# Performance work log

Measured on AMD Instinct MI355X. Metric: run time of the kernel, lower is better.

## Reference

```python
import jax, jax.numpy as jnp
import numpy as np

B = 16384
N_NEIGH = 50
D = 64
NUM_USERS = 100000
NUM_ITEMS = 100000
NUM_ENTITIES = 200000


def setup_inputs() -> dict:
    key = jax.random.key(0)
    ks = jax.random.split(key, 16)
    s = 1.0 / np.sqrt(D)
    return {
        "user_indices": jax.random.randint(ks[0], (B,), 0, NUM_USERS),
        "item_indices": jax.random.randint(ks[1], (B,), 0, NUM_ITEMS),
        "kg_adj_batch": jax.random.randint(ks[2], (B, N_NEIGH), 0, NUM_ENTITIES),
        "user_table": jax.random.normal(ks[3], (NUM_USERS, D), jnp.float32),
        "item_table": jax.random.normal(ks[4], (NUM_ITEMS, D), jnp.float32),
        "entity_table": jax.random.normal(ks[5], (NUM_ENTITIES, D), jnp.float32),
        "attn_W": jax.random.normal(ks[6], (2 * D, 1), jnp.float32) * s,
        "attn_b": jnp.zeros((1,), jnp.float32),
        "kg_W1": jax.random.normal(ks[7], (D, D), jnp.float32) * s,
        "kg_b1": jnp.zeros((D,), jnp.float32),
        "kg_W2": jax.random.normal(ks[8], (D, D), jnp.float32) * s,
        "kg_b2": jnp.zeros((D,), jnp.float32),
        "comb_W": jax.random.normal(ks[9], (2 * D, D), jnp.float32) * s,
        "comb_b": jnp.zeros((D,), jnp.float32),
        "out_W": jax.random.normal(ks[10], (2 * D, 1), jnp.float32) * s,
        "out_b": jnp.zeros((1,), jnp.float32),
    }


def reference(user_indices, item_indices, kg_adj_batch,
              user_table, item_table, entity_table,
              attn_W, attn_b, kg_W1, kg_b1, kg_W2, kg_b2,
              comb_W, comb_b, out_W, out_b):
    user_emb = user_table[user_indices]          # [B, D]
    item_emb = item_table[item_indices]          # [B, D]
    nbr_idx = jnp.clip(kg_adj_batch, 0)
    neighbor_emb = entity_table[nbr_idx]         # [B, N, D]
    # attention_linear(cat([item, nbr])) == item @ Wi + nbr @ Wn + b (avoids [B,N,2D])
    Wi, Wn = attn_W[:D], attn_W[D:]
    attn_scores = item_emb @ Wi + jnp.einsum('bnd,do->bno', neighbor_emb, Wn)[..., 0] + attn_b  # [B, N]
    attn_scores = jax.nn.leaky_relu(attn_scores, negative_slope=0.2)
    attn_weights = jax.nn.softmax(attn_scores, axis=1)                 # softmax over neighbors
    neighbor_attn = jnp.einsum('bn,bnd->bd', attn_weights, neighbor_emb)
    refined_kg = jax.nn.relu(neighbor_attn @ kg_W1 + kg_b1) @ kg_W2 + kg_b2
    combined_item = jnp.concatenate([item_emb, refined_kg], axis=1)
    final_item_rep = jax.nn.relu(combined_item @ comb_W + comb_b)      # dropout = identity (eval)
    combined_user_item = jnp.concatenate([user_emb, final_item_rep], axis=1)
    score = (combined_user_item @ out_W + out_b)[:, 0]
    return score
```

## Files before the change

### kernel.cpp

```cpp
#include <hip/hip_runtime.h>

#define NN 50
#define D 64
#define GRP 10

typedef unsigned int uint32;
typedef unsigned short ushort16;

__device__ __forceinline__ float wave_sum64(float x) {
#pragma unroll
  for (int off = 32; off > 0; off >>= 1)
    x += __shfl_xor(x, off, 64);
  return x;
}

__device__ __forceinline__ float readlane_f(float v, int l) {
  return __uint_as_float(__builtin_amdgcn_readlane(__float_as_uint(v), l));
}

__device__ __forceinline__ ushort16 f32_to_bf16(float f) {
  uint32 u = __float_as_uint(f);
  u += 0x7FFF + ((u >> 16) & 1);
  return (ushort16)(u >> 16);
}

__global__ __launch_bounds__(256, 4) void ent_proj(
    const float* __restrict__ ent_tab, const float* __restrict__ attn_W,
    float* __restrict__ proj, ushort16* __restrict__ ent_bf, int rows)
{
  const int  lane = threadIdx.x & 63;
  const long wave = (long)blockIdx.x * 4 + (threadIdx.x >> 6);
  const long base = wave * GRP;
  if (base >= rows) return;
  const float Wn = attn_W[D + lane];
  float v[GRP];
#pragma unroll
  for (int i = 0; i < GRP; ++i) {
    long r = base + i; if (r > rows - 1) r = rows - 1;
    v[i] = ent_tab[r * D + lane];
  }
  float s[GRP];
#pragma unroll
  for (int i = 0; i < GRP; ++i)
    s[i] = wave_sum64(v[i] * Wn);
#pragma unroll
  for (int i = 0; i < GRP; ++i) {
    const long r = base + i;
    if (r < rows) ent_bf[r * D + lane] = f32_to_bf16(v[i]);
  }
  if (lane == 0) {
#pragma unroll
    for (int i = 0; i < GRP; ++i)
      if (base + i < rows) proj[base + i] = s[i];
  }
}

#define PGRP 5

__device__ __forceinline__ void load_pair_grp(uint32 (&buf)[PGRP],
                                              const int* __restrict__ adjb,
                                              const uint32* __restrict__ ent32,
                                              int g, int half, int sub) {
#pragma unroll
  for (int i = 0; i < PGRP; ++i) {
    const int p = g * PGRP + i;
    int t0 = adjb[2 * p + 0]; t0 = t0 < 0 ? 0 : t0;
    int t1 = adjb[2 * p + 1]; t1 = t1 < 0 ? 0 : t1;
    const int t = half ? t1 : t0;
    buf[i] = ent32[(size_t)t * 32 + sub];
  }
}

__device__ __forceinline__ void acc_pair_grp(const uint32 (&buf)[PGRP],
                                             float e, int g, int half,
                                             float& lo0, float& lo1,
                                             float& hi0, float& hi1) {
#pragma unroll
  for (int i = 0; i < PGRP; ++i) {
    const int p = g * PGRP + i;
    const float w0 = readlane_f(e, 2 * p + 0);
    const float w1 = readlane_f(e, 2 * p + 1);
    const float w  = half ? w1 : w0;
    const float lo = __uint_as_float(buf[i] << 16);
    const float hi = __uint_as_float(buf[i] & 0xFFFF0000u);
    if (i & 1) { lo1 = fmaf(w, lo, lo1); hi1 = fmaf(w, hi, hi1); }
    else       { lo0 = fmaf(w, lo, lo0); hi0 = fmaf(w, hi, hi0); }
  }
}

__global__ __launch_bounds__(256, 4) void kgat_attn2(
    const int* __restrict__ item_idx, const int* __restrict__ adj,
    const float* __restrict__ item_tab,
    const uint32* __restrict__ ent32, const float* __restrict__ proj,
    const float* __restrict__ attn_W, const float* __restrict__ attn_b,
    float* __restrict__ naws, int B)
{
  const int lane = threadIdx.x & 63;
  const int wv   = threadIdx.x >> 6;
  const int b    = blockIdx.x * 4 + wv;
  if (b >= B) return;
  const int half = lane >> 5;
  const int sub  = lane & 31;

  const int* adjb = adj + (long)b * NN;

  uint32 GA[PGRP], GB[PGRP];
  load_pair_grp(GA, adjb, ent32, 0, half, sub);
  load_pair_grp(GB, adjb, ent32, 1, half, sub);

  const float item = item_tab[(long)item_idx[b] * D + lane];
  const float base = wave_sum64(item * attn_W[lane]) + attn_b[0];

  const int myn = lane < NN ? lane : NN - 1;
  int mi = adjb[myn]; mi = mi < 0 ? 0 : mi;
  float s = proj[mi] + base;
  s = s > 0.f ? s : 0.2f * s;
  const float e = (lane < NN) ? __expf(s - 8.0f) : 0.f;
  const float denom = wave_sum64(e);

  float lo0 = 0.f, lo1 = 0.f, hi0 = 0.f, hi1 = 0.f;
  acc_pair_grp(GA, e, 0, half, lo0, lo1, hi0, hi1);
  load_pair_grp(GA, adjb, ent32, 2, half, sub);
  acc_pair_grp(GB, e, 1, half, lo0, lo1, hi0, hi1);
  load_pair_grp(GB, adjb, ent32, 3, half, sub);
  acc_pair_grp(GA, e, 2, half, lo0, lo1, hi0, hi1);
  load_pair_grp(GA, adjb, ent32, 4, half, sub);
  acc_pair_grp(GB, e, 3, half, lo0, lo1, hi0, hi1);
  acc_pair_grp(GA, e, 4, half, lo0, lo1, hi0, hi1);

  float nlo = lo0 + lo1;
  float nhi = hi0 + hi1;
  nlo += __shfl_xor(nlo, 32, 64);
  nhi += __shfl_xor(nhi, 32, 64);

  const float inv = 1.0f / denom;
  if (lane < 32) {
    float2 val = make_float2(nlo * inv, nhi * inv);
    *(float2*)(naws + (long)b * D + 2 * sub) = val;
  }
}

__global__ __launch_bounds__(256, 4) void kgat_mlp4(
    const int* __restrict__ user_idx, const int* __restrict__ item_idx,
    const float* __restrict__ user_tab, const float* __restrict__ item_tab,
    const float* __restrict__ naws,
    const float* __restrict__ W1, const float* __restrict__ b1,
    const float* __restrict__ W2, const float* __restrict__ b2,
    const float* __restrict__ cW, const float* __restrict__ cb,
    const float* __restrict__ oW, const float* __restrict__ ob,
    float* __restrict__ out, int B)
{
  __shared__ __align__(16) float s_a[4 * 4 * D];
  __shared__ __align__(16) float s_i[4 * 4 * D];

  const int lane = threadIdx.x & 63;
  const int wv   = threadIdx.x >> 6;
  const int b0   = (blockIdx.x * 4 + wv) * 4;
  if (b0 >= B) return;

  float* saA = s_a + (wv * 4 + 0) * D;
  float* saB = s_a + (wv * 4 + 1) * D;
  float* saC = s_a + (wv * 4 + 2) * D;
  float* saD = s_a + (wv * 4 + 3) * D;
  float* siA = s_i + (wv * 4 + 0) * D;
  float* siB = s_i + (wv * 4 + 1) * D;
  float* siC = s_i + (wv * 4 + 2) * D;
  float* siD = s_i + (wv * 4 + 3) * D;

  const int bA = b0 + 0 < B ? b0 + 0 : B - 1;
  const int bB = b0 + 1 < B ? b0 + 1 : B - 1;
  const int bC = b0 + 2 < B ? b0 + 2 : B - 1;
  const int bD = b0 + 3 < B ? b0 + 3 : B - 1;

  saA[lane] = naws[(long)bA * D + lane];
  saB[lane] = naws[(long)bB * D + lane];
  saC[lane] = naws[(long)bC * D + lane];
  saD[lane] = naws[(long)bD * D + lane];
  siA[lane] = item_tab[(long)item_idx[bA] * D + lane];
  siB[lane] = item_tab[(long)item_idx[bB] * D + lane];
  siC[lane] = item_tab[(long)item_idx[bC] * D + lane];
  siD[lane] = item_tab[(long)item_idx[bD] * D + lane];
  const float usA = user_tab[(long)user_idx[bA] * D + lane];
  const float usB = user_tab[(long)user_idx[bB] * D + lane];
  const float usC = user_tab[(long)user_idx[bC] * D + lane];
  const float usD = user_tab[(long)user_idx[bD] * D + lane];

  const float b1v = b1[lane];
  float hA0 = b1v, hA1 = 0.f, hB0 = b1v, hB1 = 0.f;
  float hC0 = b1v, hC1 = 0.f, hD0 = b1v, hD1 = 0.f;
#pragma unroll
  for (int d = 0; d < D; d += 4) {
    const float w0 = W1[(d + 0) * D + lane];
    const float w1 = W1[(d + 1) * D + lane];
    const float w2 = W1[(d + 2) * D + lane];
    const float w3 = W1[(d + 3) * D + lane];
    const float4 cA = *(const float4*)(saA + d);
    const float4 cB = *(const float4*)(saB + d);
    const float4 cC = *(const float4*)(saC + d);
    const float4 cD = *(const float4*)(saD + d);
    hA0 = fmaf(cA.x, w0, hA0); hA1 = fmaf(cA.y, w1, hA1);
    hA0 = fmaf(cA.z, w2, hA0); hA1 = fmaf(cA.w, w3, hA1);
    hB0 = fmaf(cB.x, w0, hB0); hB1 = fmaf(cB.y, w1, hB1);
    hB0 = fmaf(cB.z, w2, hB0); hB1 = fmaf(cB.w, w3, hB1);
    hC0 = fmaf(cC.x, w0, hC0); hC1 = fmaf(cC.y, w1, hC1);
    hC0 = fmaf(cC.z, w2, hC0); hC1 = fmaf(cC.w, w3, hC1);
    hD0 = fmaf(cD.x, w0, hD0); hD1 = fmaf(cD.y, w1, hD1);
    hD0 = fmaf(cD.z, w2, hD0); hD1 = fmaf(cD.w, w3, hD1);
  }
  saA[lane] = fmaxf(hA0 + hA1, 0.f);
  saB[lane] = fmaxf(hB0 + hB1, 0.f);
  saC[lane] = fmaxf(hC0 + hC1, 0.f);
  saD[lane] = fmaxf(hD0 + hD1, 0.f);

  const float b2v = b2[lane];
  float rA0 = b2v, rA1 = 0.f, rB0 = b2v, rB1 = 0.f;
  float rC0 = b2v, rC1 = 0.f, rD0 = b2v, rD1 = 0.f;
#pragma unroll
  for (int d = 0; d < D; d += 4) {
    const float w0 = W2[(d + 0) * D + lane];
    const float w1 = W2[(d + 1) * D + lane];
    const float w2 = W2[(d + 2) * D + lane];
    const float w3 = W2[(d + 3) * D + lane];
    const float4 cA = *(const float4*)(saA + d);
    const float4 cB = *(const float4*)(saB + d);
    const float4 cC = *(const float4*)(saC + d);
    const float4 cD = *(const float4*)(saD + d);
    rA0 = fmaf(cA.x, w0, rA0); rA1 = fmaf(cA.y, w1, rA1);
    rA0 = fmaf(cA.z, w2, rA0); rA1 = fmaf(cA.w, w3, rA1);
    rB0 = fmaf(cB.x, w0, rB0); rB1 = fmaf(cB.y, w1, rB1);
    rB0 = fmaf(cB.z, w2, rB0); rB1 = fmaf(cB.w, w3, rB1);
    rC0 = fmaf(cC.x, w0, rC0); rC1 = fmaf(cC.y, w1, rC1);
    rC0 = fmaf(cC.z, w2, rC0); rC1 = fmaf(cC.w, w3, rC1);
    rD0 = fmaf(cD.x, w0, rD0); rD1 = fmaf(cD.y, w1, rD1);
    rD0 = fmaf(cD.z, w2, rD0); rD1 = fmaf(cD.w, w3, rD1);
  }
  saA[lane] = rA0 + rA1;
  saB[lane] = rB0 + rB1;
  saC[lane] = rC0 + rC1;
  saD[lane] = rD0 + rD1;

  const float cbv = cb[lane];
  float fA0 = cbv, fA1 = 0.f, fB0 = cbv, fB1 = 0.f;
  float fC0 = cbv, fC1 = 0.f, fD0 = cbv, fD1 = 0.f;
#pragma unroll
  for (int k = 0; k < D; k += 4) {
    const float w0 = cW[(k + 0) * D + lane];
    const float w1 = cW[(k + 1) * D + lane];
    const float w2 = cW[(k + 2) * D + lane];
    const float w3 = cW[(k + 3) * D + lane];
    const float4 cA = *(const float4*)(siA + k);
    const float4 cB = *(const float4*)(siB + k);
    const float4 cC = *(const float4*)(siC + k);
    const float4 cD = *(const float4*)(siD + k);
    fA0 = fmaf(cA.x, w0, fA0); fA1 = fmaf(cA.y, w1, fA1);
    fA0 = fmaf(cA.z, w2, fA0); fA1 = fmaf(cA.w, w3, fA1);
    fB0 = fmaf(cB.x, w0, fB0); fB1 = fmaf(cB.y, w1, fB1);
    fB0 = fmaf(cB.z, w2, fB0); fB1 = fmaf(cB.w, w3, fB1);
    fC0 = fmaf(cC.x, w0, fC0); fC1 = fmaf(cC.y, w1, fC1);
    fC0 = fmaf(cC.z, w2, fC0); fC1 = fmaf(cC.w, w3, fC1);
    fD0 = fmaf(cD.x, w0, fD0); fD1 = fmaf(cD.y, w1, fD1);
    fD0 = fmaf(cD.z, w2, fD0); fD1 = fmaf(cD.w, w3, fD1);
  }
#pragma unroll
  for (int k = 0; k < D; k += 4) {
    const float w0 = cW[(D + k + 0) * D + lane];
    const float w1 = cW[(D + k + 1) * D + lane];
    const float w2 = cW[(D + k + 2) * D + lane];
    const float w3 = cW[(D + k + 3) * D + lane];
    const float4 cA = *(const float4*)(saA + k);
    const float4 cB = *(const float4*)(saB + k);
    const float4 cC = *(const float4*)(saC + k);
    const float4 cD = *(const float4*)(saD + k);
    fA0 = fmaf(cA.x, w0, fA0); fA1 = fmaf(cA.y, w1, fA1);
    fA0 = fmaf(cA.z, w2, fA0); fA1 = fmaf(cA.w, w3, fA1);
    fB0 = fmaf(cB.x, w0, fB0); fB1 = fmaf(cB.y, w1, fB1);
    fB0 = fmaf(cB.z, w2, fB0); fB1 = fmaf(cB.w, w3, fB1);
    fC0 = fmaf(cC.x, w0, fC0); fC1 = fmaf(cC.y, w1, fC1);
    fC0 = fmaf(cC.z, w2, fC0); fC1 = fmaf(cC.w, w3, fC1);
    fD0 = fmaf(cD.x, w0, fD0); fD1 = fmaf(cD.y, w1, fD1);
    fD0 = fmaf(cD.z, w2, fD0); fD1 = fmaf(cD.w, w3, fD1);
  }
  const float fA = fmaxf(fA0 + fA1, 0.f);
  const float fB = fmaxf(fB0 + fB1, 0.f);
  const float fC = fmaxf(fC0 + fC1, 0.f);
  const float fD = fmaxf(fD0 + fD1, 0.f);

  const float oWu = oW[lane];
  const float oWf = oW[D + lane];
  const float ob0 = ob[0];
  const float scA = wave_sum64(fmaf(usA, oWu, fA * oWf));
  const float scB = wave_sum64(fmaf(usB, oWu, fB * oWf));
  const float scC = wave_sum64(fmaf(usC, oWu, fC * oWf));
  const float scD = wave_sum64(fmaf(usD, oWu, fD * oWf));
  if (lane == 0) {
    out[bA] = scA + ob0;
    if (bB != bA) out[bB] = scB + ob0;
    if (bC != bB) out[bC] = scC + ob0;
    if (bD != bC) out[bD] = scD + ob0;
  }
}

__device__ __forceinline__ void load_grp(float (&buf)[GRP],
                                         const int* __restrict__ adjb,
                                         const float* __restrict__ ent_tab,
                                         int g, int lane) {
#pragma unroll
  for (int i = 0; i < GRP; ++i) {
    int t = adjb[g * GRP + i];
    t = t < 0 ? 0 : t;
    buf[i] = ent_tab[(long)t * D + lane];
  }
}

__device__ __forceinline__ void proc_grp(const float (&buf)[GRP],
                                         float Wn, float base,
                                         float& l0, float& l1, float& na) {
  float ex[GRP];
#pragma unroll
  for (int i = 0; i < GRP; ++i) {
    float t = wave_sum64(buf[i] * Wn) + base;
    t = t > 0.f ? t : 0.2f * t;
    ex[i] = __expf(t - 8.0f);
  }
#pragma unroll
  for (int i = 0; i < GRP; ++i) {
    if (i & 1) l1 += ex[i]; else l0 += ex[i];
    na = fmaf(ex[i], buf[i], na);
  }
}

__global__ __launch_bounds__(256, 4) void kgat_r3(
    const int* __restrict__ user_idx, const int* __restrict__ item_idx,
    const int* __restrict__ adj,
    const float* __restrict__ user_tab, const float* __restrict__ item_tab,
    const float* __restrict__ ent_tab,
    const float* __restrict__ attn_W, const float* __restrict__ attn_b,
    const float* __restrict__ W1, const float* __restrict__ b1,
    const float* __restrict__ W2, const float* __restrict__ b2,
    const float* __restrict__ cW, const float* __restrict__ cb,
    const float* __restrict__ oW, const float* __restrict__ ob,
    float* __restrict__ out, int B)
{
  const int lane = threadIdx.x & 63;
  const int wv   = threadIdx.x >> 6;
  const int b    = blockIdx.x * 4 + wv;
  if (b >= B) return;

  const float user = user_tab[(long)user_idx[b] * D + lane];
  const float oWu  = oW[lane];
  const float oWf  = oW[D + lane];
  const float item = item_tab[(long)item_idx[b] * D + lane];
  const float Wi   = attn_W[lane];
  const float Wn   = attn_W[D + lane];
  const float base = wave_sum64(item * Wi) + attn_b[0];
  const int* adjb = adj + b * NN;

  float na = 0.f, l0 = 0.f, l1 = 0.f;
  float A[GRP], Bv[GRP];
  load_grp(A,  adjb, ent_tab, 0, lane);
  load_grp(Bv, adjb, ent_tab, 1, lane);
  proc_grp(A,  Wn, base, l0, l1, na);
  load_grp(A,  adjb, ent_tab, 2, lane);
  proc_grp(Bv, Wn, base, l0, l1, na);
  load_grp(Bv, adjb, ent_tab, 3, lane);
  proc_grp(A,  Wn, base, l0, l1, na);
  load_grp(A,  adjb, ent_tab, 4, lane);
  proc_grp(Bv, Wn, base, l0, l1, na);
  proc_grp(A,  Wn, base, l0, l1, na);
  na /= (l0 + l1);

  float h0 = b1[lane], h1 = 0.f, h2 = 0.f, h3 = 0.f;
#pragma unroll
  for (int d = 0; d < D; d += 4) {
    h0 = fmaf(readlane_f(na, d + 0), W1[(d + 0) * D + lane], h0);
    h1 = fmaf(readlane_f(na, d + 1), W1[(d + 1) * D + lane], h1);
    h2 = fmaf(readlane_f(na, d + 2), W1[(d + 2) * D + lane], h2);
    h3 = fmaf(readlane_f(na, d + 3), W1[(d + 3) * D + lane], h3);
  }
  const float h = fmaxf((h0 + h1) + (h2 + h3), 0.f);

  float r0 = b2[lane], r1 = 0.f, r2 = 0.f, r3 = 0.f;
#pragma unroll
  for (int d = 0; d < D; d += 4) {
    r0 = fmaf(readlane_f(h, d + 0), W2[(d + 0) * D + lane], r0);
    r1 = fmaf(readlane_f(h, d + 1), W2[(d + 1) * D + lane], r1);
    r2 = fmaf(readlane_f(h, d + 2), W2[(d + 2) * D + lane], r2);
    r3 = fmaf(readlane_f(h, d + 3), W2[(d + 3) * D + lane], r3);
  }
  const float r = (r0 + r1) + (r2 + r3);

  float f0 = cb[lane], f1 = 0.f, f2 = 0.f, f3 = 0.f;
#pragma unroll
  for (int k = 0; k < D; k += 4) {
    f0 = fmaf(readlane_f(item, k + 0), cW[(k + 0) * D + lane], f0);
    f1 = fmaf(readlane_f(item, k + 1), cW[(k + 1) * D + lane], f1);
    f2 = fmaf(readlane_f(item, k + 2), cW[(k + 2) * D + lane], f2);
    f3 = fmaf(readlane_f(item, k + 3), cW[(k + 3) * D + lane], f3);
  }
#pragma unroll
  for (int k = 0; k < D; k += 4) {
    f0 = fmaf(readlane_f(r, k + 0), cW[(D + k + 0) * D + lane], f0);
    f1 = fmaf(readlane_f(r, k + 1), cW[(D + k + 1) * D + lane], f1);
    f2 = fmaf(readlane_f(r, k + 2), cW[(D + k + 2) * D + lane], f2);
    f3 = fmaf(readlane_f(r, k + 3), cW[(D + k + 3) * D + lane], f3);
  }
  const float f = fmaxf((f0 + f1) + (f2 + f3), 0.f);

  const float sc = wave_sum64(fmaf(user, oWu, f * oWf));
  if (lane == 0) out[b] = sc + ob[0];
}

extern "C" void kernel_launch(void* const* d_in, const int* in_sizes, int n_in,
                              void* d_out, int out_size, void* d_ws, size_t ws_size,
                              hipStream_t stream) {
  const int*   user_idx = (const int*)d_in[0];
  const int*   item_idx = (const int*)d_in[1];
  const int*   adj      = (const int*)d_in[2];
  const float* user_tab = (const float*)d_in[3];
  const float* item_tab = (const float*)d_in[4];
  const float* ent_tab  = (const float*)d_in[5];
  const float* attn_W   = (const float*)d_in[6];
  const float* attn_b   = (const float*)d_in[7];
  const float* W1       = (const float*)d_in[8];
  const float* b1       = (const float*)d_in[9];
  const float* W2       = (const float*)d_in[10];
  const float* b2       = (const float*)d_in[11];
  const float* cW       = (const float*)d_in[12];
  const float* cb       = (const float*)d_in[13];
  const float* oW       = (const float*)d_in[14];
  const float* ob       = (const float*)d_in[15];
  float* out = (float*)d_out;

  const int B    = in_sizes[0];
  const int rows = in_sizes[5] / D;

  const size_t off_bf = ((size_t)rows * 4 + 255) & ~(size_t)255;
  const size_t off_na = (off_bf + (size_t)rows * D * 2 + 255) & ~(size_t)255;
  const size_t need   = off_na + (size_t)B * D * 4;

  if (ws_size >= need) {
    float*    proj   = (float*)d_ws;
    ushort16* ent_bf = (ushort16*)((char*)d_ws + off_bf);
    float*    naws   = (float*)((char*)d_ws + off_na);
    const int waves   = (rows + GRP - 1) / GRP;
    const int pblocks = (waves + 3) / 4;
    const int ablocks = (B + 3) / 4;
    const int mblocks = (B + 15) / 16;
    ent_proj<<<pblocks, 256, 0, stream>>>(ent_tab, attn_W, proj, ent_bf, rows);
    kgat_attn2<<<ablocks, 256, 0, stream>>>(item_idx, adj, item_tab,
                                            (const uint32*)ent_bf, proj,
                                            attn_W, attn_b, naws, B);
    kgat_mlp4<<<mblocks, 256, 0, stream>>>(user_idx, item_idx, user_tab,
                                           item_tab, naws, W1, b1, W2, b2,
                                           cW, cb, oW, ob, out, B);
  } else {
    const int blocks = (B + 3) / 4;
    kgat_r3<<<blocks, 256, 0, stream>>>(user_idx, item_idx, adj,
                                        user_tab, item_tab, ent_tab,
                                        attn_W, attn_b, W1, b1, W2, b2,
                                        cW, cb, oW, ob, out, B);
  }
}
```

Measured before the change: 57.63 us.

## Fold W2 into combine weights and read MLP inputs directly from global

```diff
diff --git a/kernel.cpp b/kernel.cpp
--- a/kernel.cpp
+++ b/kernel.cpp
@@ -24,34 +24,56 @@
   return (ushort16)(u >> 16);
 }
 
-__global__ __launch_bounds__(256, 4) void ent_proj(
+__global__ __launch_bounds__(256, 4) void kgat_prep(
     const float* __restrict__ ent_tab, const float* __restrict__ attn_W,
-    float* __restrict__ proj, ushort16* __restrict__ ent_bf, int rows)
+    float* __restrict__ proj, ushort16* __restrict__ ent_bf, int rows,
+    int pblocks,
+    const float* __restrict__ W2, const float* __restrict__ b2,
+    const float* __restrict__ cW, const float* __restrict__ cb,
+    float* __restrict__ W2cW, float* __restrict__ cb2)
 {
-  const int  lane = threadIdx.x & 63;
-  const long wave = (long)blockIdx.x * 4 + (threadIdx.x >> 6);
-  const long base = wave * GRP;
-  if (base >= rows) return;
-  const float Wn = attn_W[D + lane];
-  float v[GRP];
-#pragma unroll
-  for (int i = 0; i < GRP; ++i) {
-    long r = base + i; if (r > rows - 1) r = rows - 1;
-    v[i] = ent_tab[r * D + lane];
-  }
-  float s[GRP];
-#pragma unroll
-  for (int i = 0; i < GRP; ++i)
-    s[i] = wave_sum64(v[i] * Wn);
-#pragma unroll
-  for (int i = 0; i < GRP; ++i) {
-    const long r = base + i;
-    if (r < rows) ent_bf[r * D + lane] = f32_to_bf16(v[i]);
-  }
-  if (lane == 0) {
+  const int lane = threadIdx.x & 63;
+  const int wv   = threadIdx.x >> 6;
+
+  if ((int)blockIdx.x < pblocks) {
+    const long wave = (long)blockIdx.x * 4 + wv;
+    const long base = wave * GRP;
+    if (base >= rows) return;
+    const float Wn = attn_W[D + lane];
+    float v[GRP];
+#pragma unroll
+    for (int i = 0; i < GRP; ++i) {
+      long r = base + i; if (r > rows - 1) r = rows - 1;
+      v[i] = ent_tab[r * D + lane];
+    }
+    float s[GRP];
 #pragma unroll
     for (int i = 0; i < GRP; ++i)
-      if (base + i < rows) proj[base + i] = s[i];
+      s[i] = wave_sum64(v[i] * Wn);
+#pragma unroll
+    for (int i = 0; i < GRP; ++i) {
+      const long r = base + i;
+      if (r < rows) ent_bf[r * D + lane] = f32_to_bf16(v[i]);
+    }
+    if (lane == 0) {
+#pragma unroll
+      for (int i = 0; i < GRP; ++i)
+        if (base + i < rows) proj[base + i] = s[i];
+    }
+  } else {
+    const int d = ((int)blockIdx.x - pblocks) * 4 + wv;
+    float acc = 0.f;
+#pragma unroll 8
+    for (int k = 0; k < D; ++k)
+      acc = fmaf(W2[d * D + k], cW[(D + k) * D + lane], acc);
+    W2cW[d * D + lane] = acc;
+    if (d == 0) {
+      float a2 = 0.f;
+#pragma unroll 8
+      for (int k = 0; k < D; ++k)
+        a2 = fmaf(b2[k], cW[(D + k) * D + lane], a2);
+      cb2[lane] = cb[lane] + a2;
+    }
   }
 }
 
@@ -140,46 +162,50 @@
   }
 }
 
-__global__ __launch_bounds__(256, 4) void kgat_mlp4(
+__global__ __launch_bounds__(256, 4) void kgat_mlpf(
     const int* __restrict__ user_idx, const int* __restrict__ item_idx,
     const float* __restrict__ user_tab, const float* __restrict__ item_tab,
     const float* __restrict__ naws,
     const float* __restrict__ W1, const float* __restrict__ b1,
-    const float* __restrict__ W2, const float* __restrict__ b2,
-    const float* __restrict__ cW, const float* __restrict__ cb,
+    const float* __restrict__ cW,
+    const float* __restrict__ W2cW, const float* __restrict__ cb2,
     const float* __restrict__ oW, const float* __restrict__ ob,
     float* __restrict__ out, int B)
 {
-  __shared__ __align__(16) float s_a[4 * 4 * D];
-  __shared__ __align__(16) float s_i[4 * 4 * D];
+  __shared__ __align__(16) float s_h[4 * 4 * D];
 
   const int lane = threadIdx.x & 63;
   const int wv   = threadIdx.x >> 6;
   const int b0   = (blockIdx.x * 4 + wv) * 4;
   if (b0 >= B) return;
 
-  float* saA = s_a + (wv * 4 + 0) * D;
-  float* saB = s_a + (wv * 4 + 1) * D;
-  float* saC = s_a + (wv * 4 + 2) * D;
-  float* saD = s_a + (wv * 4 + 3) * D;
-  float* siA = s_i + (wv * 4 + 0) * D;
-  float* siB = s_i + (wv * 4 + 1) * D;
-  float* siC = s_i + (wv * 4 + 2) * D;
-  float* siD = s_i + (wv * 4 + 3) * D;
+  float* shA = s_h + (wv * 4 + 0) * D;
+  float* shB = s_h + (wv * 4 + 1) * D;
+  float* shC = s_h + (wv * 4 + 2) * D;
+  float* shD = s_h + (wv * 4 + 3) * D;
 
   const int bA = b0 + 0 < B ? b0 + 0 : B - 1;
   const int bB = b0 + 1 < B ? b0 + 1 : B - 1;
   const int bC = b0 + 2 < B ? b0 + 2 : B - 1;
   const int bD = b0 + 3 < B ? b0 + 3 : B - 1;
 
-  saA[lane] = naws[(long)bA * D + lane];
-  saB[lane] = naws[(long)bB * D + lane];
-  saC[lane] = naws[(long)bC * D + lane];
-  saD[lane] = naws[(long)bD * D + lane];
-  siA[lane] = item_tab[(long)item_idx[bA] * D + lane];
-  siB[lane] = item_tab[(long)item_idx[bB] * D + lane];
-  siC[lane] = item_tab[(long)item_idx[bC] * D + lane];
-  siD[lane] = item_tab[(long)item_idx[bD] * D + lane];
+  const int uA = __builtin_amdgcn_readfirstlane(bA);
+  const int uB = __builtin_amdgcn_readfirstlane(bB);
+  const int uC = __builtin_amdgcn_readfirstlane(bC);
+  const int uD = __builtin_amdgcn_readfirstlane(bD);
+  const float* napA = naws + (long)uA * D;
+  const float* napB = naws + (long)uB * D;
+  const float* napC = naws + (long)uC * D;
+  const float* napD = naws + (long)uD * D;
+  const int iiA = __builtin_amdgcn_readfirstlane(item_idx[bA]);
+  const int iiB = __builtin_amdgcn_readfirstlane(item_idx[bB]);
+  const int iiC = __builtin_amdgcn_readfirstlane(item_idx[bC]);
+  const int iiD = __builtin_amdgcn_readfirstlane(item_idx[bD]);
+  const float* itpA = item_tab + (long)iiA * D;
+  const float* itpB = item_tab + (long)iiB * D;
+  const float* itpC = item_tab + (long)iiC * D;
+  const float* itpD = item_tab + (long)iiD * D;
+
   const float usA = user_tab[(long)user_idx[bA] * D + lane];
   const float usB = user_tab[(long)user_idx[bB] * D + lane];
   const float usC = user_tab[(long)user_idx[bC] * D + lane];
@@ -194,83 +220,56 @@
     const float w1 = W1[(d + 1) * D + lane];
     const float w2 = W1[(d + 2) * D + lane];
     const float w3 = W1[(d + 3) * D + lane];
-    const float4 cA = *(const float4*)(saA + d);
-    const float4 cB = *(const float4*)(saB + d);
-    const float4 cC = *(const float4*)(saC + d);
-    const float4 cD = *(const float4*)(saD + d);
-    hA0 = fmaf(cA.x, w0, hA0); hA1 = fmaf(cA.y, w1, hA1);
-    hA0 = fmaf(cA.z, w2, hA0); hA1 = fmaf(cA.w, w3, hA1);
-    hB0 = fmaf(cB.x, w0, hB0); hB1 = fmaf(cB.y, w1, hB1);
-    hB0 = fmaf(cB.z, w2, hB0); hB1 = fmaf(cB.w, w3, hB1);
-    hC0 = fmaf(cC.x, w0, hC0); hC1 = fmaf(cC.y, w1, hC1);
-    hC0 = fmaf(cC.z, w2, hC0); hC1 = fmaf(cC.w, w3, hC1);
-    hD0 = fmaf(cD.x, w0, hD0); hD1 = fmaf(cD.y, w1, hD1);
-    hD0 = fmaf(cD.z, w2, hD0); hD1 = fmaf(cD.w, w3, hD1);
-  }
-  saA[lane] = fmaxf(hA0 + hA1, 0.f);
-  saB[lane] = fmaxf(hB0 + hB1, 0.f);
-  saC[lane] = fmaxf(hC0 + hC1, 0.f);
-  saD[lane] = fmaxf(hD0 + hD1, 0.f);
-
-  const float b2v = b2[lane];
-  float rA0 = b2v, rA1 = 0.f, rB0 = b2v, rB1 = 0.f;
-  float rC0 = b2v, rC1 = 0.f, rD0 = b2v, rD1 = 0.f;
+    const float4 aA = *(const float4*)(napA + d);
+    const float4 aB = *(const float4*)(napB + d);
+    const float4 aC = *(const float4*)(napC + d);
+    const float4 aD = *(const float4*)(napD + d);
+    hA0 = fmaf(aA.x, w0, hA0); hA1 = fmaf(aA.y, w1, hA1);
+    hA0 = fmaf(aA.z, w2, hA0); hA1 = fmaf(aA.w, w3, hA1);
+    hB0 = fmaf(aB.x, w0, hB0); hB1 = fmaf(aB.y, w1, hB1);
+    hB0 = fmaf(aB.z, w2, hB0); hB1 = fmaf(aB.w, w3, hB1);
+    hC0 = fmaf(aC.x, w0, hC0); hC1 = fmaf(aC.y, w1, hC1);
+    hC0 = fmaf(aC.z, w2, hC0); hC1 = fmaf(aC.w, w3, hC1);
+    hD0 = fmaf(aD.x, w0, hD0); hD1 = fmaf(aD.y, w1, hD1);
+    hD0 = fmaf(aD.z, w2, hD0); hD1 = fmaf(aD.w, w3, hD1);
+  }
+  shA[lane] = fmaxf(hA0 + hA1, 0.f);
+  shB[lane] = fmaxf(hB0 + hB1, 0.f);
+  shC[lane] = fmaxf(hC0 + hC1, 0.f);
+  shD[lane] = fmaxf(hD0 + hD1, 0.f);
+
+  const float cb2v = cb2[lane];
+  float fA0 = cb2v, fA1 = 0.f, fB0 = cb2v, fB1 = 0.f;
+  float fC0 = cb2v, fC1 = 0.f, fD0 = cb2v, fD1 = 0.f;
 #pragma unroll
   for (int d = 0; d < D; d += 4) {
-    const float w0 = W2[(d + 0) * D + lane];
-    const float w1 = W2[(d + 1) * D + lane];
-    const float w2 = W2[(d + 2) * D + lane];
-    const float w3 = W2[(d + 3) * D + lane];
-    const float4 cA = *(const float4*)(saA + d);
-    const float4 cB = *(const float4*)(saB + d);
-    const float4 cC = *(const float4*)(saC + d);
-    const float4 cD = *(const float4*)(saD + d);
-    rA0 = fmaf(cA.x, w0, rA0); rA1 = fmaf(cA.y, w1, rA1);
-    rA0 = fmaf(cA.z, w2, rA0); rA1 = fmaf(cA.w, w3, rA1);
-    rB0 = fmaf(cB.x, w0, rB0); rB1 = fmaf(cB.y, w1, rB1);
-    rB0 = fmaf(cB.z, w2, rB0); rB1 = fmaf(cB.w, w3, rB1);
-    rC0 = fmaf(cC.x, w0, rC0); rC1 = fmaf(cC.y, w1, rC1);
-    rC0 = fmaf(cC.z, w2, rC0); rC1 = fmaf(cC.w, w3, rC1);
-    rD0 = fmaf(cD.x, w0, rD0); rD1 = fmaf(cD.y, w1, rD1);
-    rD0 = fmaf(cD.z, w2, rD0); rD1 = fmaf(cD.w, w3, rD1);
-  }
-  saA[lane] = rA0 + rA1;
-  saB[lane] = rB0 + rB1;
-  saC[lane] = rC0 + rC1;
-  saD[lane] = rD0 + rD1;
-
-  const float cbv = cb[lane];
-  float fA0 = cbv, fA1 = 0.f, fB0 = cbv, fB1 = 0.f;
-  float fC0 = cbv, fC1 = 0.f, fD0 = cbv, fD1 = 0.f;
-#pragma unroll
-  for (int k = 0; k < D; k += 4) {
-    const float w0 = cW[(k + 0) * D + lane];
-    const float w1 = cW[(k + 1) * D + lane];
-    const float w2 = cW[(k + 2) * D + lane];
-    const float w3 = cW[(k + 3) * D + lane];
-    const float4 cA = *(const float4*)(siA + k);
-    const float4 cB = *(const float4*)(siB + k);
-    const float4 cC = *(const float4*)(siC + k);
-    const float4 cD = *(const float4*)(siD + k);
-    fA0 = fmaf(cA.x, w0, fA0); fA1 = fmaf(cA.y, w1, fA1);
-    fA0 = fmaf(cA.z, w2, fA0); fA1 = fmaf(cA.w, w3, fA1);
-    fB0 = fmaf(cB.x, w0, fB0); fB1 = fmaf(cB.y, w1, fB1);
-    fB0 = fmaf(cB.z, w2, fB0); fB1 = fmaf(cB.w, w3, fB1);
-    fC0 = fmaf(cC.x, w0, fC0); fC1 = fmaf(cC.y, w1, fC1);
-    fC0 = fmaf(cC.z, w2, fC0); fC1 = fmaf(cC.w, w3, fC1);
-    fD0 = fmaf(cD.x, w0, fD0); fD1 = fmaf(cD.y, w1, fD1);
-    fD0 = fmaf(cD.z, w2, fD0); fD1 = fmaf(cD.w, w3, fD1);
-  }
-#pragma unroll
-  for (int k = 0; k < D; k += 4) {
-    const float w0 = cW[(D + k + 0) * D + lane];
-    const float w1 = cW[(D + k + 1) * D + lane];
-    const float w2 = cW[(D + k + 2) * D + lane];
-    const float w3 = cW[(D + k + 3) * D + lane];
-    const float4 cA = *(const float4*)(saA + k);
-    const float4 cB = *(const float4*)(saB + k);
-    const float4 cC = *(const float4*)(saC + k);
-    const float4 cD = *(const float4*)(saD + k);
+    const float w0 = cW[(d + 0) * D + lane];
+    const float w1 = cW[(d + 1) * D + lane];
+    const float w2 = cW[(d + 2) * D + lane];
+    const float w3 = cW[(d + 3) * D + lane];
+    const float4 aA = *(const float4*)(itpA + d);
+    const float4 aB = *(const float4*)(itpB + d);
+    const float4 aC = *(const float4*)(itpC + d);
+    const float4 aD = *(const float4*)(itpD + d);
+    fA0 = fmaf(aA.x, w0, fA0); fA1 = fmaf(aA.y, w1, fA1);
+    fA0 = fmaf(aA.z, w2, fA0); fA1 = fmaf(aA.w, w3, fA1);
+    fB0 = fmaf(aB.x, w0, fB0); fB1 = fmaf(aB.y, w1, fB1);
+    fB0 = fmaf(aB.z, w2, fB0); fB1 = fmaf(aB.w, w3, fB1);
+    fC0 = fmaf(aC.x, w0, fC0); fC1 = fmaf(aC.y, w1, fC1);
+    fC0 = fmaf(aC.z, w2, fC0); fC1 = fmaf(aC.w, w3, fC1);
+    fD0 = fmaf(aD.x, w0, fD0); fD1 = fmaf(aD.y, w1, fD1);
+    fD0 = fmaf(aD.z, w2, fD0); fD1 = fmaf(aD.w, w3, fD1);
+  }
+#pragma unroll
+  for (int d = 0; d < D; d += 4) {
+    const float w0 = W2cW[(d + 0) * D + lane];
+    const float w1 = W2cW[(d + 1) * D + lane];
+    const float w2 = W2cW[(d + 2) * D + lane];
+    const float w3 = W2cW[(d + 3) * D + lane];
+    const float4 cA = *(const float4*)(shA + d);
+    const float4 cB = *(const float4*)(shB + d);
+    const float4 cC = *(const float4*)(shC + d);
+    const float4 cD = *(const float4*)(shD + d);
     fA0 = fmaf(cA.x, w0, fA0); fA1 = fmaf(cA.y, w1, fA1);
     fA0 = fmaf(cA.z, w2, fA0); fA1 = fmaf(cA.w, w3, fA1);
     fB0 = fmaf(cB.x, w0, fB0); fB1 = fmaf(cB.y, w1, fB1);
@@ -436,23 +435,29 @@
 
   const size_t off_bf = ((size_t)rows * 4 + 255) & ~(size_t)255;
   const size_t off_na = (off_bf + (size_t)rows * D * 2 + 255) & ~(size_t)255;
-  const size_t need   = off_na + (size_t)B * D * 4;
+  const size_t off_w2 = (off_na + (size_t)B * D * 4 + 255) & ~(size_t)255;
+  const size_t off_cb = off_w2 + (size_t)D * D * 4;
+  const size_t need   = off_cb + (size_t)D * 4;
 
   if (ws_size >= need) {
     float*    proj   = (float*)d_ws;
     ushort16* ent_bf = (ushort16*)((char*)d_ws + off_bf);
     float*    naws   = (float*)((char*)d_ws + off_na);
+    float*    W2cW   = (float*)((char*)d_ws + off_w2);
+    float*    cb2    = (float*)((char*)d_ws + off_cb);
     const int waves   = (rows + GRP - 1) / GRP;
     const int pblocks = (waves + 3) / 4;
     const int ablocks = (B + 3) / 4;
     const int mblocks = (B + 15) / 16;
-    ent_proj<<<pblocks, 256, 0, stream>>>(ent_tab, attn_W, proj, ent_bf, rows);
+    kgat_prep<<<pblocks + 16, 256, 0, stream>>>(ent_tab, attn_W, proj, ent_bf,
+                                                rows, pblocks, W2, b2, cW, cb,
+                                                W2cW, cb2);
     kgat_attn2<<<ablocks, 256, 0, stream>>>(item_idx, adj, item_tab,
                                             (const uint32*)ent_bf, proj,
                                             attn_W, attn_b, naws, B);
-    kgat_mlp4<<<mblocks, 256, 0, stream>>>(user_idx, item_idx, user_tab,
-                                           item_tab, naws, W1, b1, W2, b2,
-                                           cW, cb, oW, ob, out, B);
+    kgat_mlpf<<<mblocks, 256, 0, stream>>>(user_idx, item_idx, user_tab,
+                                           item_tab, naws, W1, b1, cW,
+                                           W2cW, cb2, oW, ob, out, B);
   } else {
     const int blocks = (B + 3) / 4;
     kgat_r3<<<blocks, 256, 0, stream>>>(user_idx, item_idx, adj,
```

After: 52.13 us. -9.6%, faster.
